# Optimization experiments

Measured on AMD Instinct MI355X. Metric: run time of the kernel, lower is better.

Reference implementation:

```python
import jax, jax.numpy as jnp
import numpy as np

N_NODES = 100000
N_EDGES = 3200000
N_GRAPHS = 4096
N_REL = 5
N_BASES = 4
HID = 32


def setup_inputs() -> dict:
    key = jax.random.key(0)
    ks = jax.random.split(key, 32)
    inp = {}
    inp['x'] = jax.random.normal(ks[0], (N_NODES, 4), dtype=jnp.float32)
    inp['edge_index'] = jax.random.randint(ks[1], (2, N_EDGES), 0, N_NODES, dtype=jnp.int64)
    inp['edge_type'] = jax.random.randint(ks[2], (N_EDGES,), 0, N_REL, dtype=jnp.int64)
    inp['user_idx'] = jax.random.randint(ks[3], (N_GRAPHS,), 0, N_NODES, dtype=jnp.int64)
    inp['item_idx'] = jax.random.randint(ks[4], (N_GRAPHS,), 0, N_NODES, dtype=jnp.int64)
    k = 5
    for l in range(4):
        in_c = 4 if l == 0 else HID
        inp[f'basis{l}'] = jax.random.normal(ks[k], (N_BASES, in_c, HID), dtype=jnp.float32) * 0.1; k += 1
        inp[f'comp{l}'] = jax.random.normal(ks[k], (N_REL, N_BASES), dtype=jnp.float32) * 0.5; k += 1
        inp[f'root{l}'] = jax.random.normal(ks[k], (in_c, HID), dtype=jnp.float32) * 0.1; k += 1
        inp[f'bias{l}'] = jax.random.normal(ks[k], (HID,), dtype=jnp.float32) * 0.01; k += 1
    inp['w1'] = jax.random.normal(ks[k], (256, 128), dtype=jnp.float32) * 0.05; k += 1
    inp['b1'] = jnp.zeros((128,), dtype=jnp.float32)
    inp['w2'] = jax.random.normal(ks[k], (128, 1), dtype=jnp.float32) * 0.05; k += 1
    inp['b2'] = jnp.zeros((1,), dtype=jnp.float32)
    return inp


def _rgcn_layer(x, src, key5, inv_cnt, basis, comp, root, bias, n_nodes):
    # mean-aggregate raw source features per (dst, relation): [N, R, in]
    agg = jax.ops.segment_sum(x[src], key5, num_segments=n_nodes * N_REL)
    agg = agg.reshape(n_nodes, N_REL, -1) * inv_cnt
    # basis-decomposed relation weights: W_r = sum_b comp[r,b] * basis[b]
    w = jnp.einsum('rb,bio->rio', comp, basis)  # [R, in, out]
    return jnp.einsum('nri,rio->no', agg, w) + x @ root + bias


def reference(x, edge_index, edge_type, user_idx, item_idx,
              basis0, comp0, root0, bias0,
              basis1, comp1, root1, bias1,
              basis2, comp2, root2, bias2,
              basis3, comp3, root3, bias3,
              w1, b1, w2, b2):
    n_nodes = x.shape[0]
    src, dst = edge_index[0], edge_index[1]
    key5 = dst * N_REL + edge_type  # combined (dst, relation) segment id
    cnt = jax.ops.segment_sum(jnp.ones_like(edge_type, dtype=x.dtype), key5,
                              num_segments=n_nodes * N_REL)
    inv_cnt = (1.0 / jnp.maximum(cnt, 1.0)).reshape(n_nodes, N_REL, 1)
    params = [(basis0, comp0, root0, bias0), (basis1, comp1, root1, bias1),
              (basis2, comp2, root2, bias2), (basis3, comp3, root3, bias3)]
    out = x
    hs = []
    for (basis, comp, root, bias) in params:
        out = jnp.tanh(_rgcn_layer(out, src, key5, inv_cnt, basis, comp, root, bias, n_nodes))
        hs.append(out)
    h = jnp.concatenate(hs, axis=1)            # [N, 128]
    g = jnp.concatenate([h[user_idx], h[item_idx]], axis=1)  # [B, 256]
    z = jax.nn.relu(g @ w1 + b1)
    return (z @ w2 + b2)[:, 0]
```

## Files before the change

kernel.cpp:

```cpp
#include <hip/hip_runtime.h>
#include <hip/hip_bf16.h>
#include <hip/hip_fp16.h>

#define N_NODES 100000
#define N_EDGES 3200000
#define N_GRAPHS 4096
#define N_REL 5
#define N_BASES 4
#define HID 32
#define SEG (N_NODES*N_REL)
#define DUMMY N_NODES

#define BNODE 196
#define NBUCK 511
#define BCAP  7168
#define PBCAP 10752
#define NKEY  980
#define PTILE 4096

#define KDIM 192
#define ASTR 208

typedef _Float16 half8 __attribute__((ext_vector_type(8)));
typedef float floatx4 __attribute__((ext_vector_type(4)));

static __global__ __launch_bounds__(256) void k_part(const int* __restrict__ ei,
                                                     const int* __restrict__ et,
                                                     int* __restrict__ gcur,
                                                     unsigned long long* __restrict__ part) {
    __shared__ unsigned long long stage[PTILE];
    __shared__ int hist[NBUCK];
    __shared__ int lofs[NBUCK];
    __shared__ int lbase[NBUCK];
    __shared__ int sscan[256];
    int t = threadIdx.x;
    int e0 = blockIdx.x * PTILE;
    int tile_n = N_EDGES - e0; if (tile_n > PTILE) tile_n = PTILE;

    for (int k = t; k < NBUCK; k += 256) hist[k] = 0;
    __syncthreads();
    int src[16], bkt[16], lkey[16];
#pragma unroll
    for (int j = 0; j < 16; j++) {
        int e = e0 + j * 256 + t;
        if (e < N_EDGES) {
            int s = ei[e];
            int d = ei[N_EDGES + e];
            int r = et[e];
            int bb = d / BNODE;
            src[j] = s; bkt[j] = bb; lkey[j] = (d - bb * BNODE) * 5 + r;
            atomicAdd(&hist[bb], 1);
        } else bkt[j] = -1;
    }
    __syncthreads();
    int h0 = (2 * t     < NBUCK) ? hist[2 * t]     : 0;
    int h1 = (2 * t + 1 < NBUCK) ? hist[2 * t + 1] : 0;
    int s2 = h0 + h1;
    sscan[t] = s2;
    __syncthreads();
    for (int off = 1; off < 256; off <<= 1) {
        int xv = (t >= off) ? sscan[t - off] : 0;
        __syncthreads();
        sscan[t] += xv;
        __syncthreads();
    }
    int excl = sscan[t] - s2;
    if (2 * t     < NBUCK) lofs[2 * t]     = excl;
    if (2 * t + 1 < NBUCK) lofs[2 * t + 1] = excl + h0;
    for (int k = t; k < NBUCK; k += 256) lbase[k] = atomicAdd(&gcur[k], hist[k]);
    __syncthreads();
    for (int k = t; k < NBUCK; k += 256) hist[k] = 0;
    __syncthreads();
#pragma unroll
    for (int j = 0; j < 16; j++) {
        if (bkt[j] >= 0) {
            int rank = atomicAdd(&hist[bkt[j]], 1);
            stage[lofs[bkt[j]] + rank] =
                ((unsigned long long)(unsigned)((bkt[j] << 16) | lkey[j]) << 32)
                | (unsigned)src[j];
        }
    }
    __syncthreads();
    for (int i = t; i < tile_n; i += 256) {
        unsigned long long u = stage[i];
        unsigned hi = (unsigned)(u >> 32);
        int bb = hi >> 16;
        unsigned long long lk = hi & 0xFFFFu;
        int pos = lbase[bb] + (i - lofs[bb]);
        if (pos < BCAP)
            part[(size_t)bb * BCAP + pos] = (lk << 32) | (u & 0xffffffffULL);
    }
}

static __global__ __launch_bounds__(1024) void k_bsort(const unsigned long long* __restrict__ part,
                                                       const int* __restrict__ gcur,
                                                       int* __restrict__ offs,
                                                       int* __restrict__ cnt,
                                                       int* __restrict__ srcs) {
    __shared__ int lhist[NKEY];
    __shared__ int lscan[NKEY];
    __shared__ int sscan[256];
    __shared__ int lsrc[PBCAP];
    int b = blockIdx.x;
    int t = threadIdx.x;
    int n = gcur[b]; if (n > BCAP) n = BCAP;
    const unsigned long long* reg = part + (size_t)b * BCAP;

    for (int k = t; k < NKEY; k += 1024) lhist[k] = 0;
    __syncthreads();
    for (int i = t; i < n; i += 1024)
        atomicAdd(&lhist[(int)(reg[i] >> 32)], 1);
    __syncthreads();

    int loc[5]; int s5 = 0;
    if (t < 196) {
#pragma unroll
        for (int j = 0; j < 5; j++) { loc[j] = s5; s5 += (lhist[t * 5 + j] + 7) & ~7; }
    }
    if (t < 256) sscan[t] = (t < 196) ? s5 : 0;
    __syncthreads();
    for (int off = 1; off < 256; off <<= 1) {
        int x = (t >= off && t < 256) ? sscan[t - off] : 0;
        __syncthreads();
        if (t < 256) sscan[t] += x;
        __syncthreads();
    }
    if (t < 196) {
        int excl = sscan[t] - s5;
#pragma unroll
        for (int j = 0; j < 5; j++) lscan[t * 5 + j] = excl + loc[j];
    }
    __syncthreads();
    int ptot = sscan[255]; if (ptot > PBCAP) ptot = PBCAP;
    int pout = ptot + 16; if (pout > PBCAP) pout = PBCAP;

    int base = b * PBCAP;
    if (t < 196) {
#pragma unroll
        for (int j = 0; j < 5; j++) {
            int k = t * 5 + j;
            int segid = b * NKEY + k;
            if (segid < SEG) {
                cnt[segid]  = lhist[k];
                offs[segid] = base + lscan[k];
            }
        }
    }
    __syncthreads();
    for (int k = t; k < NKEY; k += 1024) lhist[k] = 0;
    for (int i = t; i < pout; i += 1024) lsrc[i] = DUMMY;
    __syncthreads();
    for (int i = t; i < n; i += 1024) {
        unsigned long long u = reg[i];
        int k = (int)(u >> 32);
        int pos = lscan[k] + atomicAdd(&lhist[k], 1);
        if (pos < PBCAP) lsrc[pos] = (int)(u & 0xffffffffULL);
    }
    __syncthreads();
    for (int i = t; i < pout; i += 1024) srcs[base + i] = lsrc[i];
}

static __global__ __launch_bounds__(256) void k_prep(
    const float* __restrict__ x,
    __half* __restrict__ ht0, __half* __restrict__ ht1, __half* __restrict__ ht2,
    __half* __restrict__ ht3, __half* __restrict__ ht4, int* __restrict__ srcs,
    const float* __restrict__ ba0, const float* __restrict__ co0, const float* __restrict__ ro0,
    const float* __restrict__ ba1, const float* __restrict__ co1, const float* __restrict__ ro1,
    const float* __restrict__ ba2, const float* __restrict__ co2, const float* __restrict__ ro2,
    const float* __restrict__ ba3, const float* __restrict__ co3, const float* __restrict__ ro3,
    __half* __restrict__ Wb, const float* __restrict__ w1, __half* __restrict__ Wm) {
    int blk = blockIdx.x;
    int t = threadIdx.x;
    if (blk < 12501) {
        int tid = blk * 256 + t;
        if (tid < (N_NODES + 1) * 32) {
            int nd = tid >> 5, ii = tid & 31;
            float v = (nd < N_NODES && ii < 4) ? x[(nd << 2) + ii] : 0.f;
            ht0[tid] = __float2half(v);
        } else {
            int r = tid - (N_NODES + 1) * 32;
            if (r < 128) {
                __half* hp = (r < 32) ? ht1 : (r < 64) ? ht2 : (r < 96) ? ht3 : ht4;
                hp[N_NODES * 32 + (r & 31)] = __float2half(0.f);
            } else if (r < 144) srcs[NBUCK * PBCAP + (r - 128)] = DUMMY;
        }
    } else if (blk < 12501 + 96) {
        int idx = (blk - 12501) * 256 + t;
        int j    = idx & 7;
        int lane = (idx >> 3) & 63;
        int tile = (idx >> 9) & 1;
        int ls   = idx >> 10;
        int l    = ls / 6;
        int s    = ls - l * 6;
        const float* basis = (l == 0) ? ba0 : (l == 1) ? ba1 : (l == 2) ? ba2 : ba3;
        const float* comp  = (l == 0) ? co0 : (l == 1) ? co1 : (l == 2) ? co2 : co3;
        const float* root  = (l == 0) ? ro0 : (l == 1) ? ro1 : (l == 2) ? ro2 : ro3;
        int in_c = (l == 0) ? 4 : HID;
        int d = ((lane >> 4) << 3) + j;
        int o = tile * 16 + (lane & 15);
        float v = 0.f;
        if (d < in_c) {
            if (s < 5) {
                float acc = 0.f;
#pragma unroll
                for (int b = 0; b < N_BASES; b++)
                    acc += comp[s * N_BASES + b] * basis[(b * in_c + d) * HID + o];
                v = acc;
            } else {
                v = root[d * HID + o];
            }
        }
        Wb[idx] = __float2half(v);
    } else {
        int idx = (blk - 12597) * 256 + t;
        int j    = idx & 7;
        int lane = (idx >> 3) & 63;
        int s    = (idx >> 9) & 7;
        int tile = idx >> 12;
        int k = s * 32 + ((lane >> 4) << 3) + j;
        int o = tile * 16 + (lane & 15);
        Wm[idx] = __float2half(w1[k * 128 + o]);
    }
}

static __global__ __launch_bounds__(128, 5) void k_layer(
    const __half* __restrict__ tab, const int* __restrict__ offs,
    const int* __restrict__ cnt, const int* __restrict__ srcs,
    const __half* __restrict__ Wbl, const float* __restrict__ bias,
    __half* __restrict__ hout) {
    __shared__ __align__(16) __half sAgg[32 * ASTR];
    int t = threadIdx.x;
    int wave = t >> 6, lane = t & 63;
    int nsub = lane >> 2, cp = lane & 3;
    int nl = wave * 16 + nsub;
    int n = blockIdx.x * 32 + nl;
    const half8* tab8 = (const half8*)tab;

    int s5 = n * N_REL;
    int o0 = offs[s5];
    int cc[5];
#pragma unroll
    for (int r = 0; r < 5; r++) cc[r] = cnt[s5 + r];

    __half* row = sAgg + nl * ASTR;
    *(half8*)(row + 160 + cp * 8) = tab8[n * 4 + cp];

    int ob[5];
    {
        int orun = o0;
#pragma unroll
        for (int r = 0; r < 5; r++) { ob[r] = orun; orun += (cc[r] + 7) & ~7; }
    }
    int4 E0[5], E1[5];
#pragma unroll
    for (int r = 0; r < 5; r++) {
        const int* sp = srcs + ob[r];
        E0[r] = *(const int4*)(sp);
        E1[r] = *(const int4*)(sp + 4);
    }
#pragma unroll
    for (int r = 0; r < 5; r++) {
        int cr = cc[r];
        int pr = (cr + 7) & ~7;
        const int* sp = srcs + ob[r];
        half8 g0 = tab8[E0[r].x * 4 + cp], g1 = tab8[E0[r].y * 4 + cp];
        half8 g2 = tab8[E0[r].z * 4 + cp], g3 = tab8[E0[r].w * 4 + cp];
        half8 g4 = tab8[E1[r].x * 4 + cp], g5 = tab8[E1[r].y * 4 + cp];
        half8 g6 = tab8[E1[r].z * 4 + cp], g7 = tab8[E1[r].w * 4 + cp];
        half8 sb = ((g0 + g1) + (g2 + g3)) + ((g4 + g5) + (g6 + g7));
        float S0 = (float)sb[0], S1 = (float)sb[1], S2 = (float)sb[2], S3 = (float)sb[3];
        float S4 = (float)sb[4], S5 = (float)sb[5], S6 = (float)sb[6], S7 = (float)sb[7];
        for (int s8 = 8; s8 < pr; s8 += 8) {
            int4 f0 = *(const int4*)(sp + s8);
            int4 f1 = *(const int4*)(sp + s8 + 4);
            half8 h0 = tab8[f0.x * 4 + cp], h1 = tab8[f0.y * 4 + cp];
            half8 h2 = tab8[f0.z * 4 + cp], h3 = tab8[f0.w * 4 + cp];
            half8 h4 = tab8[f1.x * 4 + cp], h5 = tab8[f1.y * 4 + cp];
            half8 h6 = tab8[f1.z * 4 + cp], h7 = tab8[f1.w * 4 + cp];
            half8 rb = ((h0 + h1) + (h2 + h3)) + ((h4 + h5) + (h6 + h7));
            S0 += (float)rb[0]; S1 += (float)rb[1]; S2 += (float)rb[2]; S3 += (float)rb[3];
            S4 += (float)rb[4]; S5 += (float)rb[5]; S6 += (float)rb[6]; S7 += (float)rb[7];
        }
        float ic = (cr > 0) ? __builtin_amdgcn_rcpf((float)cr) : 0.f;
        half8 u;
        u[0] = (_Float16)(S0 * ic); u[1] = (_Float16)(S1 * ic);
        u[2] = (_Float16)(S2 * ic); u[3] = (_Float16)(S3 * ic);
        u[4] = (_Float16)(S4 * ic); u[5] = (_Float16)(S5 * ic);
        u[6] = (_Float16)(S6 * ic); u[7] = (_Float16)(S7 * ic);
        *(half8*)(row + r * 32 + cp * 8) = u;
    }
    __syncthreads();

    floatx4 acc0 = {0.f, 0.f, 0.f, 0.f}, acc1 = {0.f, 0.f, 0.f, 0.f};
    const __half* aBase = sAgg + (wave * 16 + (lane & 15)) * ASTR + ((lane >> 4) << 3);
    const __half* bBase = Wbl + lane * 8;
#pragma unroll
    for (int s = 0; s < 6; s++) {
        half8 a  = *(const half8*)(aBase + s * 32);
        half8 f0 = *(const half8*)(bBase + (s * 2 + 0) * 512);
        half8 f1 = *(const half8*)(bBase + (s * 2 + 1) * 512);
        acc0 = __builtin_amdgcn_mfma_f32_16x16x32_f16(a, f0, acc0, 0, 0, 0);
        acc1 = __builtin_amdgcn_mfma_f32_16x16x32_f16(a, f1, acc1, 0, 0, 0);
    }
    int oc = lane & 15;
    float bi0 = bias[oc], bi1 = bias[16 + oc];
#pragma unroll
    for (int r = 0; r < 4; r++) {
        int node = blockIdx.x * 32 + wave * 16 + ((lane >> 4) << 2) + r;
        hout[node * 32 + oc]      = __float2half(tanhf(acc0[r] + bi0));
        hout[node * 32 + 16 + oc] = __float2half(tanhf(acc1[r] + bi1));
    }
}

static __global__ __launch_bounds__(256) void k_mlp(
    const __half* __restrict__ h1, const __half* __restrict__ h2,
    const __half* __restrict__ h3, const __half* __restrict__ h4,
    const int* __restrict__ uidx, const int* __restrict__ iidx,
    const __half* __restrict__ Wm, const float* __restrict__ b1,
    const float* __restrict__ w2, const float* __restrict__ b2,
    float* __restrict__ out) {
    __shared__ __align__(16) __half sg[16 * 264];
    __shared__ float sacc[4][16];
    int t = threadIdx.x, wave = t >> 6, lane = t & 63;
    int g0 = blockIdx.x * 16;
    int lt = lane >> 4, lp = lane & 15;
    const __half* htab = (lt == 0) ? h1 : (lt == 1) ? h2 : (lt == 2) ? h3 : h4;
#pragma unroll
    for (int gg2 = 0; gg2 < 4; gg2++) {
        int gg = wave * 4 + gg2;
        int g = g0 + gg;
        int u = uidx[g], it = iidx[g];
        __half2* dst = (__half2*)(sg + gg * 264);
        dst[lt * 16 + lp]      = ((const __half2*)(htab + u * 32))[lp];
        dst[64 + lt * 16 + lp] = ((const __half2*)(htab + it * 32))[lp];
    }
    __syncthreads();
    floatx4 acc0 = {0.f, 0.f, 0.f, 0.f}, acc1 = {0.f, 0.f, 0.f, 0.f};
    const __half* aBase = sg + (lane & 15) * 264 + ((lane >> 4) << 3);
    const __half* bB0 = Wm + (wave * 2 + 0) * 4096 + lane * 8;
    const __half* bB1 = Wm + (wave * 2 + 1) * 4096 + lane * 8;
#pragma unroll
    for (int s = 0; s < 8; s++) {
        half8 a  = *(const half8*)(aBase + s * 32);
        half8 f0 = *(const half8*)(bB0 + s * 512);
        half8 f1 = *(const half8*)(bB1 + s * 512);
        acc0 = __builtin_amdgcn_mfma_f32_16x16x32_f16(a, f0, acc0, 0, 0, 0);
        acc1 = __builtin_amdgcn_mfma_f32_16x16x32_f16(a, f1, acc1, 0, 0, 0);
    }
    int o0 = wave * 32 + (lane & 15);
    int o1 = o0 + 16;
    float b10 = b1[o0], b11 = b1[o1], w20 = w2[o0], w21 = w2[o1];
#pragma unroll
    for (int r = 0; r < 4; r++) {
        float z0 = fmaxf(acc0[r] + b10, 0.f);
        float z1 = fmaxf(acc1[r] + b11, 0.f);
        float v = z0 * w20 + z1 * w21;
#pragma unroll
        for (int off = 1; off < 16; off <<= 1) v += __shfl_xor(v, off);
        if ((lane & 15) == 0) sacc[wave][((lane >> 4) << 2) + r] = v;
    }
    __syncthreads();
    if (t < 16)
        out[g0 + t] = sacc[0][t] + sacc[1][t] + sacc[2][t] + sacc[3][t] + b2[0];
}

extern "C" void kernel_launch(void* const* d_in, const int* in_sizes, int n_in,
                              void* d_out, int out_size, void* d_ws, size_t ws_size,
                              hipStream_t stream) {
    const float* x  = (const float*)d_in[0];
    const int*   ei = (const int*)d_in[1];
    const int*   et = (const int*)d_in[2];
    const int*   ui = (const int*)d_in[3];
    const int*   ii = (const int*)d_in[4];
    const float* w1 = (const float*)d_in[21];
    const float* b1 = (const float*)d_in[22];
    const float* w2 = (const float*)d_in[23];
    const float* b2 = (const float*)d_in[24];

    char* ws = (char*)d_ws;
    if (ws_size < 92167680UL) return;
    int*    gcur = (int*)(ws + 0);
    int*    offs = (int*)(ws + 2048);
    int*    cnt  = (int*)(ws + 2002176);
    int*    srcs = (int*)(ws + 4002304);
    __half* Wb   = (__half*)(ws + 26079488);
    __half* Wm   = (__half*)(ws + 26128640);
    __half* ht0  = (__half*)(ws + 26194176);
    __half* ht1  = (__half*)(ws + 32594304);
    __half* ht2  = (__half*)(ws + 38994432);
    __half* ht3  = (__half*)(ws + 45394560);
    __half* ht4  = (__half*)(ws + 51794688);
    unsigned long long* part = (unsigned long long*)(ws + 32594304);

    hipMemsetAsync(gcur, 0, NBUCK * 4, stream);

    k_part<<<(N_EDGES + PTILE - 1) / PTILE, 256, 0, stream>>>(ei, et, gcur, part);
    k_bsort<<<NBUCK, 1024, 0, stream>>>(part, gcur, offs, cnt, srcs);
    k_prep<<<12725, 256, 0, stream>>>(
        x, ht0, ht1, ht2, ht3, ht4, srcs,
        (const float*)d_in[5],  (const float*)d_in[6],  (const float*)d_in[7],
        (const float*)d_in[9],  (const float*)d_in[10], (const float*)d_in[11],
        (const float*)d_in[13], (const float*)d_in[14], (const float*)d_in[15],
        (const float*)d_in[17], (const float*)d_in[18], (const float*)d_in[19],
        Wb, w1, Wm);

    __half* tabs[5] = {ht0, ht1, ht2, ht3, ht4};
    for (int l = 0; l < 4; l++) {
        const float* bias = (const float*)d_in[8 + 4 * l];
        k_layer<<<N_NODES / 32, 128, 0, stream>>>(
            tabs[l], offs, cnt, srcs, Wb + l * 6144, bias, tabs[l + 1]);
    }
    k_mlp<<<256, 256, 0, stream>>>(ht1, ht2, ht3, ht4, ui, ii, Wm, b1, w2, b2,
                                   (float*)d_out);
}
```

Measured before the change: 339.5 us.

## Specialize first RGCN layer on compact 4-wide fp16 input and shrink blocks

Layer 0 no longer gathers from a 32-wide zero-padded fp16 table. A new k_layer0 reads a compact 4-channel fp16 copy of x, where each of the 4 lanes per node gathers a different edge's half4, and the partial sums are combined with lane shuffles. This cuts gather traffic for the first layer and shrinks the prep kernel that built the padded table. All layer kernels also move from 128-thread, 32-node blocks to 64-thread, 16-node blocks for finer scheduling, which means more blocks and more per-block overhead.

```diff
diff --git a/kernel.cpp b/kernel.cpp
--- a/kernel.cpp
+++ b/kernel.cpp
@@ -22,7 +22,19 @@
 #define ASTR 208
 
 typedef _Float16 half8 __attribute__((ext_vector_type(8)));
+typedef _Float16 half4 __attribute__((ext_vector_type(4)));
 typedef float floatx4 __attribute__((ext_vector_type(4)));
+
+__device__ inline half4 qshfl_xor(half4 v, int m) {
+    union U { half4 h; long long l; } u; u.h = v;
+    u.l = __shfl_xor(u.l, m);
+    return u.h;
+}
+__device__ inline int qsel(int cp, int4 v) {
+    int a = (cp & 1) ? v.y : v.x;
+    int b = (cp & 1) ? v.w : v.z;
+    return (cp & 2) ? b : a;
+}
 
 static __global__ __launch_bounds__(256) void k_part(const int* __restrict__ ei,
                                                      const int* __restrict__ et,
@@ -161,8 +173,8 @@
 }
 
 static __global__ __launch_bounds__(256) void k_prep(
-    const float* __restrict__ x,
-    __half* __restrict__ ht0, __half* __restrict__ ht1, __half* __restrict__ ht2,
+    const float* __restrict__ x, __half* __restrict__ xt,
+    __half* __restrict__ ht1, __half* __restrict__ ht2,
     __half* __restrict__ ht3, __half* __restrict__ ht4, int* __restrict__ srcs,
     const float* __restrict__ ba0, const float* __restrict__ co0, const float* __restrict__ ro0,
     const float* __restrict__ ba1, const float* __restrict__ co1, const float* __restrict__ ro1,
@@ -171,21 +183,19 @@
     __half* __restrict__ Wb, const float* __restrict__ w1, __half* __restrict__ Wm) {
     int blk = blockIdx.x;
     int t = threadIdx.x;
-    if (blk < 12501) {
+    if (blk < 1563) {
         int tid = blk * 256 + t;
-        if (tid < (N_NODES + 1) * 32) {
-            int nd = tid >> 5, ii = tid & 31;
-            float v = (nd < N_NODES && ii < 4) ? x[(nd << 2) + ii] : 0.f;
-            ht0[tid] = __float2half(v);
-        } else {
-            int r = tid - (N_NODES + 1) * 32;
-            if (r < 128) {
-                __half* hp = (r < 32) ? ht1 : (r < 64) ? ht2 : (r < 96) ? ht3 : ht4;
-                hp[N_NODES * 32 + (r & 31)] = __float2half(0.f);
-            } else if (r < 144) srcs[NBUCK * PBCAP + (r - 128)] = DUMMY;
-        }
-    } else if (blk < 12501 + 96) {
-        int idx = (blk - 12501) * 256 + t;
+        if (tid < (N_NODES + 1) * 4) {
+            float v = (tid < N_NODES * 4) ? x[tid] : 0.f;
+            xt[tid] = __float2half(v);
+        }
+    } else if (blk == 1563) {
+        if (t < 128) {
+            __half* hp = (t < 32) ? ht1 : (t < 64) ? ht2 : (t < 96) ? ht3 : ht4;
+            hp[N_NODES * 32 + (t & 31)] = __float2half(0.f);
+        } else if (t < 144) srcs[NBUCK * PBCAP + (t - 128)] = DUMMY;
+    } else if (blk < 1564 + 96) {
+        int idx = (blk - 1564) * 256 + t;
         int j    = idx & 7;
         int lane = (idx >> 3) & 63;
         int tile = (idx >> 9) & 1;
@@ -212,7 +222,7 @@
         }
         Wb[idx] = __float2half(v);
     } else {
-        int idx = (blk - 12597) * 256 + t;
+        int idx = (blk - 1660) * 256 + t;
         int j    = idx & 7;
         int lane = (idx >> 3) & 63;
         int s    = (idx >> 9) & 7;
@@ -223,17 +233,105 @@
     }
 }
 
-static __global__ __launch_bounds__(128, 5) void k_layer(
+static __global__ __launch_bounds__(64, 6) void k_layer0(
+    const __half* __restrict__ xt, const int* __restrict__ offs,
+    const int* __restrict__ cnt, const int* __restrict__ srcs,
+    const __half* __restrict__ Wbl, const float* __restrict__ bias,
+    __half* __restrict__ hout) {
+    __shared__ __align__(16) __half sAgg[16 * ASTR];
+    int lane = threadIdx.x;
+    int nsub = lane >> 2, cp = lane & 3;
+    int n = blockIdx.x * 16 + nsub;
+    const half4* xt4 = (const half4*)xt;
+
+    half8 z = {};
+    for (int i = lane; i < 16 * ASTR / 8; i += 64) ((half8*)sAgg)[i] = z;
+
+    int s5 = n * N_REL;
+    int o0 = offs[s5];
+    int cc[5];
+#pragma unroll
+    for (int r = 0; r < 5; r++) cc[r] = cnt[s5 + r];
+    int ob[5];
+    {
+        int orun = o0;
+#pragma unroll
+        for (int r = 0; r < 5; r++) { ob[r] = orun; orun += (cc[r] + 7) & ~7; }
+    }
+    int4 E0[5], E1[5];
+#pragma unroll
+    for (int r = 0; r < 5; r++) {
+        const int* sp = srcs + ob[r];
+        E0[r] = *(const int4*)(sp);
+        E1[r] = *(const int4*)(sp + 4);
+    }
+    half4 selfv = xt4[n];
+    __syncthreads();
+
+    __half* row = sAgg + nsub * ASTR;
+    if (cp == 0) *(half4*)(row + 160) = selfv;
+
+#pragma unroll
+    for (int r = 0; r < 5; r++) {
+        int cr = cc[r];
+        int pr = (cr + 7) & ~7;
+        const int* sp = srcs + ob[r];
+        half4 xa = xt4[qsel(cp, E0[r])];
+        half4 xb = xt4[qsel(cp, E1[r])];
+        half4 hs = xa + xb;
+        hs += qshfl_xor(hs, 1);
+        hs += qshfl_xor(hs, 2);
+        float S0 = (float)hs[0], S1 = (float)hs[1], S2 = (float)hs[2], S3 = (float)hs[3];
+        for (int s8 = 8; s8 < pr; s8 += 8) {
+            int4 f0 = *(const int4*)(sp + s8);
+            int4 f1 = *(const int4*)(sp + s8 + 4);
+            half4 ya = xt4[qsel(cp, f0)];
+            half4 yb = xt4[qsel(cp, f1)];
+            half4 rs = ya + yb;
+            rs += qshfl_xor(rs, 1);
+            rs += qshfl_xor(rs, 2);
+            S0 += (float)rs[0]; S1 += (float)rs[1]; S2 += (float)rs[2]; S3 += (float)rs[3];
+        }
+        float ic = (cr > 0) ? __builtin_amdgcn_rcpf((float)cr) : 0.f;
+        if (cp == 0) {
+            half4 u;
+            u[0] = (_Float16)(S0 * ic); u[1] = (_Float16)(S1 * ic);
+            u[2] = (_Float16)(S2 * ic); u[3] = (_Float16)(S3 * ic);
+            *(half4*)(row + r * 32) = u;
+        }
+    }
+    __syncthreads();
+
+    floatx4 acc0 = {0.f, 0.f, 0.f, 0.f}, acc1 = {0.f, 0.f, 0.f, 0.f};
+    const __half* aBase = sAgg + (lane & 15) * ASTR + ((lane >> 4) << 3);
+    const __half* bBase = Wbl + lane * 8;
+#pragma unroll
+    for (int s = 0; s < 6; s++) {
+        half8 a  = *(const half8*)(aBase + s * 32);
+        half8 f0 = *(const half8*)(bBase + (s * 2 + 0) * 512);
+        half8 f1 = *(const half8*)(bBase + (s * 2 + 1) * 512);
+        acc0 = __builtin_amdgcn_mfma_f32_16x16x32_f16(a, f0, acc0, 0, 0, 0);
+        acc1 = __builtin_amdgcn_mfma_f32_16x16x32_f16(a, f1, acc1, 0, 0, 0);
+    }
+    int oc = lane & 15;
+    float bi0 = bias[oc], bi1 = bias[16 + oc];
+#pragma unroll
+    for (int r = 0; r < 4; r++) {
+        int node = blockIdx.x * 16 + ((lane >> 4) << 2) + r;
+        hout[node * 32 + oc]      = __float2half(tanhf(acc0[r] + bi0));
+        hout[node * 32 + 16 + oc] = __float2half(tanhf(acc1[r] + bi1));
+    }
+}
+
+static __global__ __launch_bounds__(64, 6) void k_layer(
     const __half* __restrict__ tab, const int* __restrict__ offs,
     const int* __restrict__ cnt, const int* __restrict__ srcs,
     const __half* __restrict__ Wbl, const float* __restrict__ bias,
     __half* __restrict__ hout) {
-    __shared__ __align__(16) __half sAgg[32 * ASTR];
-    int t = threadIdx.x;
-    int wave = t >> 6, lane = t & 63;
+    __shared__ __align__(16) __half sAgg[16 * ASTR];
+    int lane = threadIdx.x;
     int nsub = lane >> 2, cp = lane & 3;
-    int nl = wave * 16 + nsub;
-    int n = blockIdx.x * 32 + nl;
+    int n = blockIdx.x * 16 + nsub;
     const half8* tab8 = (const half8*)tab;
 
     int s5 = n * N_REL;
@@ -242,7 +340,7 @@
 #pragma unroll
     for (int r = 0; r < 5; r++) cc[r] = cnt[s5 + r];
 
-    __half* row = sAgg + nl * ASTR;
+    __half* row = sAgg + nsub * ASTR;
     *(half8*)(row + 160 + cp * 8) = tab8[n * 4 + cp];
 
     int ob[5];
@@ -292,7 +390,7 @@
     __syncthreads();
 
     floatx4 acc0 = {0.f, 0.f, 0.f, 0.f}, acc1 = {0.f, 0.f, 0.f, 0.f};
-    const __half* aBase = sAgg + (wave * 16 + (lane & 15)) * ASTR + ((lane >> 4) << 3);
+    const __half* aBase = sAgg + (lane & 15) * ASTR + ((lane >> 4) << 3);
     const __half* bBase = Wbl + lane * 8;
 #pragma unroll
     for (int s = 0; s < 6; s++) {
@@ -306,7 +404,7 @@
     float bi0 = bias[oc], bi1 = bias[16 + oc];
 #pragma unroll
     for (int r = 0; r < 4; r++) {
-        int node = blockIdx.x * 32 + wave * 16 + ((lane >> 4) << 2) + r;
+        int node = blockIdx.x * 16 + ((lane >> 4) << 2) + r;
         hout[node * 32 + oc]      = __float2half(tanhf(acc0[r] + bi0));
         hout[node * 32 + 16 + oc] = __float2half(tanhf(acc1[r] + bi1));
     }
@@ -385,30 +483,32 @@
     int*    srcs = (int*)(ws + 4002304);
     __half* Wb   = (__half*)(ws + 26079488);
     __half* Wm   = (__half*)(ws + 26128640);
-    __half* ht0  = (__half*)(ws + 26194176);
-    __half* ht1  = (__half*)(ws + 32594304);
-    __half* ht2  = (__half*)(ws + 38994432);
-    __half* ht3  = (__half*)(ws + 45394560);
-    __half* ht4  = (__half*)(ws + 51794688);
-    unsigned long long* part = (unsigned long long*)(ws + 32594304);
+    __half* xt   = (__half*)(ws + 26194176);
+    __half* ht1  = (__half*)(ws + 26994304);
+    __half* ht2  = (__half*)(ws + 33394432);
+    __half* ht3  = (__half*)(ws + 39794560);
+    __half* ht4  = (__half*)(ws + 46194688);
+    unsigned long long* part = (unsigned long long*)(ws + 26994304);
 
     hipMemsetAsync(gcur, 0, NBUCK * 4, stream);
 
     k_part<<<(N_EDGES + PTILE - 1) / PTILE, 256, 0, stream>>>(ei, et, gcur, part);
     k_bsort<<<NBUCK, 1024, 0, stream>>>(part, gcur, offs, cnt, srcs);
-    k_prep<<<12725, 256, 0, stream>>>(
-        x, ht0, ht1, ht2, ht3, ht4, srcs,
+    k_prep<<<1788, 256, 0, stream>>>(
+        x, xt, ht1, ht2, ht3, ht4, srcs,
         (const float*)d_in[5],  (const float*)d_in[6],  (const float*)d_in[7],
         (const float*)d_in[9],  (const float*)d_in[10], (const float*)d_in[11],
         (const float*)d_in[13], (const float*)d_in[14], (const float*)d_in[15],
         (const float*)d_in[17], (const float*)d_in[18], (const float*)d_in[19],
         Wb, w1, Wm);
 
-    __half* tabs[5] = {ht0, ht1, ht2, ht3, ht4};
-    for (int l = 0; l < 4; l++) {
+    k_layer0<<<N_NODES / 16, 64, 0, stream>>>(
+        xt, offs, cnt, srcs, Wb, (const float*)d_in[8], ht1);
+    __half* tabs[4] = {ht1, ht2, ht3, ht4};
+    for (int l = 1; l < 4; l++) {
         const float* bias = (const float*)d_in[8 + 4 * l];
-        k_layer<<<N_NODES / 32, 128, 0, stream>>>(
-            tabs[l], offs, cnt, srcs, Wb + l * 6144, bias, tabs[l + 1]);
+        k_layer<<<N_NODES / 16, 64, 0, stream>>>(
+            tabs[l - 1], offs, cnt, srcs, Wb + l * 6144, bias, tabs[l]);
     }
     k_mlp<<<256, 256, 0, stream>>>(ht1, ht2, ht3, ht4, ui, ii, Wm, b1, w2, b2,
                                    (float*)d_out);
```

Result: slower. 347.3 us (+2.3%).
